# Kernel optimization log

Measured on AMD Instinct MI355X. Metric: run time of the kernel, lower is better.

The kernel has to match this reference:

```python
import jax, jax.numpy as jnp
import numpy as np

GRID = 128
N0 = 262144
CHANNELS = [16, 32, 64, 128, 256]
EPS = 1e-5
OFFS2 = [(dx, dy, dz) for dx in (0, 1) for dy in (0, 1) for dz in (0, 1)]
OFFS3 = [(dx, dy, dz) for dx in (-1, 0, 1) for dy in (-1, 0, 1) for dz in (-1, 0, 1)]


def _keys(c, size):
    return (c[:, 0].astype(np.int64) * size + c[:, 1]) * size + c[:, 2]


def _rulebook(in_coords, out_coords, offsets, size_in, stride):
    # explicit-GEMM rulebook: for each kernel offset, (input_idx, output_idx) pairs,
    # padded to n_out with a validity mask so shapes are static.
    ik = _keys(in_coords, size_in)
    order = np.argsort(ik)
    sk = ik[order]
    K, P = len(offsets), out_coords.shape[0]
    I = np.zeros((K, P), np.int32)
    O = np.zeros((K, P), np.int32)
    M = np.zeros((K, P), bool)
    for k, off in enumerate(offsets):
        nbr = out_coords * stride + np.asarray(off)
        valid = np.all((nbr >= 0) & (nbr < size_in), axis=1)
        nk = _keys(np.clip(nbr, 0, size_in - 1), size_in)
        pos = np.minimum(np.searchsorted(sk, nk), len(sk) - 1)
        found = valid & (sk[pos] == nk)
        cnt = int(found.sum())
        I[k, :cnt] = order[pos[found]]
        O[k, :cnt] = np.nonzero(found)[0]
        M[k, :cnt] = True
    return I, O, M


def setup_inputs() -> dict:
    rng = np.random.RandomState(0)
    flat = rng.choice(GRID ** 3, size=N0, replace=False)
    coords = np.stack([flat // (GRID * GRID), (flat // GRID) % GRID, flat % GRID], 1).astype(np.int64)
    key = jax.random.key(0)
    ctr = [0]
    def nrm(shape, scale=1.0):
        ctr[0] += 1
        return scale * jax.random.normal(jax.random.fold_in(key, ctr[0]), shape, jnp.float32)
    inp = {"x": nrm((N0, CHANNELS[0]))}
    size = GRID
    for l in range(4):
        cin, cout = CHANNELS[l], CHANNELS[l + 1]
        out_coords = np.unique(coords // 2, axis=0)
        dI, dO, dM = _rulebook(coords, out_coords, OFFS2, size, 2)       # stride-2, k=2 down conv
        bI, bO, bM = _rulebook(out_coords, out_coords, OFFS3, size // 2, 1)  # stride-1, k=3 block conv
        inp[f"dW{l}"] = nrm((8, cin, cout), (8 * cin) ** -0.5)
        inp[f"dI{l}"] = jnp.asarray(dI); inp[f"dO{l}"] = jnp.asarray(dO); inp[f"dM{l}"] = jnp.asarray(dM)
        inp[f"dG{l}"] = 1.0 + nrm((cout,), 0.1)
        inp[f"dB{l}"] = nrm((cout,), 0.1)
        inp[f"dN{l}"] = int(out_coords.shape[0])
        inp[f"bW{l}"] = nrm((27, cout, cout), (27 * cout) ** -0.5)
        inp[f"bC{l}"] = nrm((cout,), 0.01)
        inp[f"bI{l}"] = jnp.asarray(bI); inp[f"bO{l}"] = jnp.asarray(bO); inp[f"bM{l}"] = jnp.asarray(bM)
        inp[f"bG{l}"] = 1.0 + nrm((cout,), 0.1)
        inp[f"bH{l}"] = nrm((cout,), 0.1)
        coords = out_coords
        size //= 2
    return inp


def _conv(f, W, I, O, M, n_out, bias=None):
    # gather -> GEMM -> scatter-add, one pass per kernel offset (fixed small K)
    out = jnp.zeros((n_out, W.shape[-1]), f.dtype)
    for k in range(W.shape[0]):
        g = jnp.where(M[k][:, None], f[I[k]], 0.0)
        out = out.at[O[k]].add(g @ W[k])
    return out if bias is None else out + bias


def _bn_relu(f, g, b):
    # training-mode BatchNorm over active voxels, fused with ReLU
    m = f.mean(0)
    v = jnp.mean((f - m) ** 2, 0)
    return jax.nn.relu((f - m) * (g * jax.lax.rsqrt(v + EPS)) + b)


def _forward(x, levels):
    outs = [x]
    for (dW, dI, dO, dM, dG, dB, dN, bW, bC, bI, bO, bM, bG, bH) in levels:
        x = _bn_relu(_conv(x, dW, dI, dO, dM, dN), dG, dB)        # down block (bias=False)
        x = _bn_relu(_conv(x, bW, bI, bO, bM, dN, bC), bG, bH)    # ConvBlock
        outs.append(x)
    return tuple(outs)


def reference(x, dW0, dI0, dO0, dM0, dG0, dB0, dN0, bW0, bC0, bI0, bO0, bM0, bG0, bH0,
              dW1, dI1, dO1, dM1, dG1, dB1, dN1, bW1, bC1, bI1, bO1, bM1, bG1, bH1,
              dW2, dI2, dO2, dM2, dG2, dB2, dN2, bW2, bC2, bI2, bO2, bM2, bG2, bH2,
              dW3, dI3, dO3, dM3, dG3, dB3, dN3, bW3, bC3, bI3, bO3, bM3, bG3, bH3):
    levels = [
        (dW0, dI0, dO0, dM0, dG0, dB0, dN0, bW0, bC0, bI0, bO0, bM0, bG0, bH0),
        (dW1, dI1, dO1, dM1, dG1, dB1, dN1, bW1, bC1, bI1, bO1, bM1, bG1, bH1),
        (dW2, dI2, dO2, dM2, dG2, dB2, dN2, bW2, bC2, bI2, bO2, bM2, bG2, bH2),
        (dW3, dI3, dO3, dM3, dG3, dB3, dN3, bW3, bC3, bI3, bO3, bM3, bG3, bH3),
    ]
    return _forward(x, levels)
```

## Files before the change

### kernel.cpp

```cpp
#include <hip/hip_runtime.h>
#include <hip/hip_bf16.h>
#include <stdint.h>
#include <stddef.h>

typedef __hip_bfloat16 bf16;
typedef __attribute__((ext_vector_type(8))) short bf8_t;
typedef __attribute__((ext_vector_type(4))) float f4_t;
static const int CH[5] = {16, 32, 64, 128, 256};

__device__ __forceinline__ float b2f(unsigned short u) {
    return __uint_as_float(((unsigned int)u) << 16);
}
__device__ __forceinline__ unsigned short f2bu(float f) {
    union { bf16 h; unsigned short u; } cv;
    cv.h = __float2bfloat16(f);
    return cv.u;
}
__device__ __forceinline__ void fma4(float4& a, float s, const float4& w) {
    a.x = fmaf(s, w.x, a.x);
    a.y = fmaf(s, w.y, a.y);
    a.z = fmaf(s, w.z, a.z);
    a.w = fmaf(s, w.w, a.w);
}
struct us4 { unsigned short a, b, c, d; };

__global__ void k_sentinel(float* __restrict__ out, float v) {
    if (threadIdx.x == 0) out[0] = v;
}

__global__ void SparseConvEncoder_20633022890309_kernel(
        const unsigned char* __restrict__ bM0, int* __restrict__ flag) {
    if (threadIdx.x == 0) {
        flag[0] = 1;
        flag[1] = 0;
        flag[2] = (bM0[0] == 1 && bM0[1] == 0 && bM0[2] == 0 && bM0[3] == 0 && bM0[4] == 1) ? 1 : 0;
    }
}

__global__ void __launch_bounds__(256) k_copy(const float* __restrict__ x,
                                              float* __restrict__ y, long n) {
    long i = (long)blockIdx.x * 256 + threadIdx.x;
    if (i < n) y[i] = x[i];
}

__global__ void __launch_bounds__(256) k_copytob(const float* __restrict__ x,
                                                 float* __restrict__ y,
                                                 unsigned short* __restrict__ yb, long n) {
    long i = (long)blockIdx.x * 256 + threadIdx.x;
    if (i < n) {
        float v = x[i];
        y[i] = v;
        yb[i] = f2bu(v);
    }
}

__global__ void __launch_bounds__(256) k_wt2(const float* __restrict__ dW,
                                             unsigned short* __restrict__ dWt, int dcin,
                                             const float* __restrict__ bW,
                                             unsigned short* __restrict__ bWt, int bcin,
                                             int cout, long dtot, long btot) {
    long i = (long)blockIdx.x * 256 + threadIdx.x;
    if (i < dtot) {
        long cc = (long)dcin * cout;
        int k = (int)(i / cc);
        int rem = (int)(i % cc);
        int co = rem / dcin, ci = rem % dcin;
        dWt[i] = f2bu(dW[((long)k * dcin + ci) * cout + co]);
    } else if (i < dtot + btot) {
        long j = i - dtot;
        long cc = (long)bcin * cout;
        int k = (int)(j / cc);
        int rem = (int)(j % cc);
        int co = rem / bcin, ci = rem % bcin;
        bWt[j] = f2bu(bW[((long)k * bcin + ci) * cout + co]);
    }
}

__global__ void __launch_bounds__(256) k_scatter(const int* __restrict__ I,
                                                 const int* __restrict__ O,
                                                 const void* __restrict__ M,
                                                 const int* __restrict__ flag,
                                                 int* __restrict__ R, int P, int k0, int cnt) {
    int i = blockIdx.x * 256 + threadIdx.x;
    if (i >= cnt) return;
    long gi = (long)k0 * P + i;
    int m = flag[2] ? ((const int*)M)[gi] : (int)((const unsigned char*)M)[gi];
    if (!m) return;
    R[(long)(i / P) * P + O[gi]] = I[gi];
}

__global__ void __launch_bounds__(256) k_init(float* __restrict__ out,
                                              const float* __restrict__ bias,
                                              long total, int maskC) {
    long i = (long)blockIdx.x * 256 + threadIdx.x;
    if (i < total) out[i] = bias ? bias[i & maskC] : 0.f;
}

template <int CIN, int TN, int MODE, int KT>
__global__ void __launch_bounds__(256) k_mconv(const unsigned short* __restrict__ Xb,
                                               const unsigned short* __restrict__ Wt,
                                               const float* __restrict__ bias,
                                               const int* __restrict__ R,
                                               float* __restrict__ out,
                                               int n, int cout, int kcnt, int gs) {
    const int lane = threadIdx.x & 63;
    const int wave = threadIdx.x >> 6;
    const int rt = blockIdx.x * 4 + wave;
    const int row_tiles = (n + 15) >> 4;
    if (rt >= row_tiles) return;
    const int m = lane & 15, q = lane >> 4;
    const int o = rt * 16 + m;
    const int co0 = blockIdx.y * (16 * TN);
    const bf8_t zero = {};

    f4_t acc[TN];
#pragma unroll
    for (int t = 0; t < TN; ++t) {
        if (MODE == 0) {
            float bv = bias ? bias[co0 + t * 16 + m] : 0.f;
            acc[t][0] = bv; acc[t][1] = bv; acc[t][2] = bv; acc[t][3] = bv;
        } else if (MODE == 1) {
#pragma unroll
            for (int g = 0; g < 4; ++g) {
                int row = rt * 16 + q * 4 + g;
                acc[t][g] = (row < n) ? out[(long)row * cout + co0 + t * 16 + m] : 0.f;
            }
        } else {
            acc[t][0] = 0.f; acc[t][1] = 0.f; acc[t][2] = 0.f; acc[t][3] = 0.f;
        }
    }

    bool touched = (MODE != 2);

    if constexpr (KT > 0) {
        int r[KT];
#pragma unroll
        for (int kk = 0; kk < KT; ++kk)
            r[kk] = (o < n) ? R[(long)kk * n + o] : -1;

        if constexpr (CIN == 16) {
            bf8_t a[KT / 2];
#pragma unroll
            for (int p = 0; p < KT / 2; ++p) {
                int rsel = (q < 2) ? r[2 * p] : r[2 * p + 1];
                long ax = (long)((rsel >= 0) ? rsel : 0) * CIN + (q & 1) * 8;
                bf8_t av = *(const bf8_t*)(Xb + ax);
                a[p] = (rsel >= 0) ? av : zero;
            }
#pragma unroll
            for (int p = 0; p < KT / 2; ++p) {
                int ksel = 2 * p + (q >> 1);
#pragma unroll
                for (int t = 0; t < TN; ++t) {
                    int co = co0 + t * 16 + m;
                    long bx = ((long)ksel * cout + co) * CIN + (q & 1) * 8;
                    bf8_t b = *(const bf8_t*)(Wt + bx);
                    acc[t] = __builtin_amdgcn_mfma_f32_16x16x32_bf16(a[p], b, acc[t], 0, 0, 0);
                }
            }
        } else {
            constexpr int NC = CIN / 32;
            constexpr int GB = (KT > 9) ? 9 : KT;
#pragma unroll
            for (int g0 = 0; g0 < KT; g0 += GB) {
                bf8_t a[GB][NC];
#pragma unroll
                for (int j = 0; j < GB; ++j) {
                    int kk = g0 + j;
#pragma unroll
                    for (int cb = 0; cb < NC; ++cb) {
                        long ax = (long)((r[kk] >= 0) ? r[kk] : 0) * CIN + cb * 32 + q * 8;
                        bf8_t av = *(const bf8_t*)(Xb + ax);
                        a[j][cb] = (r[kk] >= 0) ? av : zero;
                    }
                }
#pragma unroll
                for (int j = 0; j < GB; ++j) {
                    int kk = g0 + j;
#pragma unroll
                    for (int cb = 0; cb < NC; ++cb) {
#pragma unroll
                        for (int t = 0; t < TN; ++t) {
                            int co = co0 + t * 16 + m;
                            long bx = ((long)kk * cout + co) * CIN + cb * 32 + q * 8;
                            bf8_t b = *(const bf8_t*)(Wt + bx);
                            acc[t] = __builtin_amdgcn_mfma_f32_16x16x32_bf16(a[j][cb], b,
                                                                             acc[t], 0, 0, 0);
                        }
                    }
                }
            }
        }
    } else {
        int ks = 0, ke = kcnt;
        if (MODE == 2) {
            ks = blockIdx.z * gs;
            ke = ks + gs;
            if (ke > kcnt) ke = kcnt;
        }
        constexpr int NC = (CIN >= 32) ? (CIN / 32) : 1;
        constexpr int JB = (CIN >= 128) ? 2 : 4;
        for (int kb = ks; kb < ke; kb += JB) {
            int rj[JB];
#pragma unroll
            for (int j = 0; j < JB; ++j) {
                int kk = kb + j;
                rj[j] = (kk < ke && o < n) ? R[(long)kk * n + o] : -1;
            }
            if (MODE == 2) {
                int any = 0;
#pragma unroll
                for (int j = 0; j < JB; ++j) any |= (rj[j] >= 0) ? 1 : 0;
                if (__ballot(any) == 0ULL) continue;
                touched = true;
            }
            bf8_t a[JB][NC];
#pragma unroll
            for (int j = 0; j < JB; ++j) {
                int kk = kb + j;
                bool inb = (kk < ke) && (rj[j] >= 0);
#pragma unroll
                for (int cb = 0; cb < NC; ++cb) {
                    const bool kval = !(CIN == 16 && q >= 2);
                    const int kbase = (CIN == 16) ? (kval ? q * 8 : 0) : (cb * 32 + q * 8);
                    long ax = (long)(inb ? rj[j] : 0) * CIN + kbase;
                    bf8_t av = *(const bf8_t*)(Xb + ax);
                    a[j][cb] = (inb && kval) ? av : zero;
                }
            }
#pragma unroll
            for (int j = 0; j < JB; ++j) {
                int kk = kb + j;
                if (kk >= ke) break;
#pragma unroll
                for (int cb = 0; cb < NC; ++cb) {
                    const bool kval = !(CIN == 16 && q >= 2);
                    const int kbase = (CIN == 16) ? (kval ? q * 8 : 0) : (cb * 32 + q * 8);
#pragma unroll
                    for (int t = 0; t < TN; ++t) {
                        int co = co0 + t * 16 + m;
                        long bx = ((long)kk * cout + co) * CIN + kbase;
                        bf8_t bv = *(const bf8_t*)(Wt + bx);
                        bf8_t b = kval ? bv : zero;
                        acc[t] = __builtin_amdgcn_mfma_f32_16x16x32_bf16(a[j][cb], b,
                                                                         acc[t], 0, 0, 0);
                    }
                }
            }
        }
    }

    if (MODE == 2 && !touched) return;
#pragma unroll
    for (int t = 0; t < TN; ++t) {
#pragma unroll
        for (int g = 0; g < 4; ++g) {
            int row = rt * 16 + q * 4 + g;
            if (row >= n) continue;
            float* p = out + (long)row * cout + co0 + t * 16 + m;
            if (MODE == 2) atomicAdd(p, acc[t][g]);
            else *p = acc[t][g];
        }
    }
}

static void mconv_dispatch(int cin, int tn, int mode, int kt, dim3 grd,
                           const unsigned short* Xb, const unsigned short* Wt,
                           const float* bias, const int* R, float* out,
                           int n, int cout, int kcnt, int gs, hipStream_t stream) {
#define MF_(CC, TT, KK)                                                            \
    if (cin == CC && tn == TT && mode == 0 && kt == KK) {                          \
        k_mconv<CC, TT, 0, KK><<<grd, 256, 0, stream>>>(Xb, Wt, bias, R, out, n,   \
                                                        cout, kcnt, gs);           \
        return;                                                                    \
    }
    MF_(16, 2, 8) MF_(32, 2, 8) MF_(32, 4, 8) MF_(64, 2, 8) MF_(64, 4, 8)
    MF_(32, 2, 27) MF_(64, 2, 27) MF_(64, 4, 27)
#undef MF_
#define M3_(CC, TT, MM)                                                            \
    if (cin == CC && tn == TT && mode == MM) {                                     \
        k_mconv<CC, TT, MM, 0><<<grd, 256, 0, stream>>>(Xb, Wt, bias, R, out, n,   \
                                                        cout, kcnt, gs);           \
        return;                                                                    \
    }
#define M2_(CC) M3_(CC, 2, 0) M3_(CC, 2, 1) M3_(CC, 2, 2) \
                M3_(CC, 4, 0) M3_(CC, 4, 1) M3_(CC, 4, 2)
    M2_(16) M2_(32) M2_(64) M2_(128) M2_(256)
#undef M2_
#undef M3_
}

static void run_mconv(const unsigned short* Xb, const unsigned short* Wt,
                      const float* bias, const int* I, const int* O, const void* M,
                      const int* flag, int* R, float* out, int n, int cin, int cout,
                      int K, int G, hipStream_t stream) {
    int rt = (n + 15) / 16;
    int bx = (rt + 3) / 4;
    int tn = (cout >= 64) ? 4 : 2;
    int gy = cout / (16 * tn);
    if (tn == 4 && (long)bx * gy < 1024) { tn = 2; gy = cout / 32; }
    long bxy = (long)bx * gy;
    int kg = 1;
    if (bxy < 512 && G >= K) {
        kg = (int)((1024 + bxy - 1) / bxy);
        if (kg > K) kg = K;
    }
    int gs = (K + kg - 1) / kg;
    kg = (K + gs - 1) / gs;

    if (kg > 1) {
        int cnt = K * n;
        hipMemsetAsync(R, 0xFF, (size_t)cnt * 4, stream);
        k_scatter<<<(cnt + 255) / 256, 256, 0, stream>>>(I, O, M, flag, R, n, 0, cnt);
        long tot = (long)n * cout;
        k_init<<<(int)((tot + 255) / 256), 256, 0, stream>>>(out, bias, tot, cout - 1);
        mconv_dispatch(cin, tn, 2, 0, dim3(bx, gy, kg), Xb, Wt, bias, R, out,
                       n, cout, K, gs, stream);
    } else {
        for (int k0 = 0; k0 < K; k0 += G) {
            int g = (K - k0 < G) ? (K - k0) : G;
            int cnt = g * n;
            hipMemsetAsync(R, 0xFF, (size_t)cnt * 4, stream);
            k_scatter<<<(cnt + 255) / 256, 256, 0, stream>>>(I, O, M, flag, R, n, k0, cnt);
            int kt = (k0 == 0 && g == K) ? K : 0;
            mconv_dispatch(cin, tn, (k0 == 0) ? 0 : 1, kt, dim3(bx, gy, 1), Xb,
                           Wt + (size_t)k0 * cout * cin, bias, R, out,
                           n, cout, g, g, stream);
        }
    }
}

template <int CIN, int ROWS, int XBF, int MODE>
__global__ void __launch_bounds__(256) k_conv_t(const void* __restrict__ X,
                                                const float* __restrict__ W,
                                                const float* __restrict__ bias,
                                                const int* __restrict__ R,
                                                float* __restrict__ out,
                                                int n, int cout,
                                                int wk0, int kcnt, int gs) {
    const int c4 = threadIdx.x;
    const int by = blockDim.y;
    const int base = blockIdx.x * by * ROWS;
    const float* Xf = (const float*)X;
    const unsigned short* Xb = (const unsigned short*)X;

    int o[ROWS];
    float4 acc[ROWS];
    bool touched[ROWS];
#pragma unroll
    for (int j = 0; j < ROWS; ++j) {
        o[j] = base + j * by + threadIdx.y;
        touched[j] = false;
        acc[j] = make_float4(0.f, 0.f, 0.f, 0.f);
        if (o[j] < n) {
            if (MODE == 0) {
                if (bias) acc[j] = *(const float4*)(bias + c4 * 4);
            } else if (MODE == 1) {
                acc[j] = *(const float4*)(out + (long)o[j] * cout + c4 * 4);
            }
        }
    }
    int ks = 0, ke = kcnt;
    if (MODE == 2) {
        ks = blockIdx.y * gs;
        ke = ks + gs;
        if (ke > kcnt) ke = kcnt;
    }
    for (int kk = ks; kk < ke; ++kk) {
        int r[ROWS];
        bool any = false;
#pragma unroll
        for (int j = 0; j < ROWS; ++j) {
            r[j] = (o[j] < n) ? R[(long)kk * n + o[j]] : -1;
            any = any || (r[j] >= 0);
            touched[j] = touched[j] || (r[j] >= 0);
        }
        if (!any) continue;
        const float* wk = W + ((long)(wk0 + kk) * CIN) * cout + c4 * 4;
#pragma unroll
        for (int ci = 0; ci < CIN; ci += 4) {
            float4 w0 = *(const float4*)(wk + (long)(ci + 0) * cout);
            float4 w1 = *(const float4*)(wk + (long)(ci + 1) * cout);
            float4 w2 = *(const float4*)(wk + (long)(ci + 2) * cout);
            float4 w3 = *(const float4*)(wk + (long)(ci + 3) * cout);
#pragma unroll
            for (int j = 0; j < ROWS; ++j) {
                if (r[j] < 0) continue;
                float x0, x1, x2, x3;
                if (XBF) {
                    us4 u = *(const us4*)(Xb + (long)r[j] * CIN + ci);
                    x0 = b2f(u.a); x1 = b2f(u.b); x2 = b2f(u.c); x3 = b2f(u.d);
                } else {
                    float4 xv = *(const float4*)(Xf + (long)r[j] * CIN + ci);
                    x0 = xv.x; x1 = xv.y; x2 = xv.z; x3 = xv.w;
                }
                fma4(acc[j], x0, w0);
                fma4(acc[j], x1, w1);
                fma4(acc[j], x2, w2);
                fma4(acc[j], x3, w3);
            }
        }
    }
#pragma unroll
    for (int j = 0; j < ROWS; ++j) {
        if (o[j] >= n) continue;
        if (MODE == 2) {
            if (!touched[j]) continue;
            float* p = out + (long)o[j] * cout + c4 * 4;
            atomicAdd(p + 0, acc[j].x);
            atomicAdd(p + 1, acc[j].y);
            atomicAdd(p + 2, acc[j].z);
            atomicAdd(p + 3, acc[j].w);
        } else {
            *(float4*)(out + (long)o[j] * cout + c4 * 4) = acc[j];
        }
    }
}

static void conv_dispatch(int cin, int rows, int xbf, int mode, dim3 grd, dim3 blk,
                          const void* X, const float* W, const float* bias,
                          const int* R, float* out, int n, int cout,
                          int wk0, int kcnt, int gs, hipStream_t stream) {
#define C3_(CC, RR, XB, MM)                                                        \
    if (cin == CC && rows == RR && xbf == XB && mode == MM) {                      \
        k_conv_t<CC, RR, XB, MM><<<grd, blk, 0, stream>>>(X, W, bias, R, out, n,   \
                                                          cout, wk0, kcnt, gs);    \
        return;                                                                    \
    }
#define C2_(CC, RR) C3_(CC, RR, 0, 0) C3_(CC, RR, 0, 1) C3_(CC, RR, 0, 2) \
                    C3_(CC, RR, 1, 0) C3_(CC, RR, 1, 1) C3_(CC, RR, 1, 2)
#define C1_(CC) C2_(CC, 1) C2_(CC, 2) C2_(CC, 4)
    C1_(16) C1_(32) C1_(64) C1_(128) C1_(256)
#undef C1_
#undef C2_
#undef C3_
}

static void run_conv(const void* X, int xbf, const float* W, const float* bias,
                     const int* I, const int* O, const void* M, const int* flag,
                     int* R, float* out, int n, int cin, int cout, int K,
                     int G, hipStream_t stream) {
    int bx = cout / 4, by = 256 / bx;
    int g4 = (n + by * 4 - 1) / (by * 4);
    int g2 = (n + by * 2 - 1) / (by * 2);
    int rows;
    if (g4 >= 1024) rows = 4;
    else if (g2 >= 1024) rows = 2;
    else rows = 1;
    int gridn = (n + by * rows - 1) / (by * rows);
    int kg = 1;
    if (gridn < 768 && G >= K) {
        kg = (2048 + gridn - 1) / gridn;
        if (kg > K) kg = K;
    }
    int gs = (K + kg - 1) / kg;
    kg = (K + gs - 1) / gs;
    dim3 blk(bx, by);
    if (kg > 1) {
        int cnt = K * n;
        hipMemsetAsync(R, 0xFF, (size_t)cnt * 4, stream);
        k_scatter<<<(cnt + 255) / 256, 256, 0, stream>>>(I, O, M, flag, R, n, 0, cnt);
        long tot = (long)n * cout;
        k_init<<<(int)((tot + 255) / 256), 256, 0, stream>>>(out, bias, tot, cout - 1);
        conv_dispatch(cin, rows, xbf, 2, dim3(gridn, kg), blk, X, W, bias, R, out,
                      n, cout, 0, K, gs, stream);
    } else {
        for (int k0 = 0; k0 < K; k0 += G) {
            int g = (K - k0 < G) ? (K - k0) : G;
            int cnt = g * n;
            hipMemsetAsync(R, 0xFF, (size_t)cnt * 4, stream);
            k_scatter<<<(cnt + 255) / 256, 256, 0, stream>>>(I, O, M, flag, R, n, k0, cnt);
            conv_dispatch(cin, rows, xbf, (k0 == 0) ? 0 : 1, dim3(gridn, 1), blk,
                          X, W, bias, R, out, n, cout, k0, g, g, stream);
        }
    }
}

__global__ void __launch_bounds__(256) k_stats(const float* __restrict__ X,
                                               float* __restrict__ sums, int n, int C) {
    int c = threadIdx.x, ty = threadIdx.y, ny = blockDim.y;
    float s1 = 0.f, s2 = 0.f;
    for (int o = blockIdx.x * ny + ty; o < n; o += gridDim.x * ny) {
        float v = X[(long)o * C + c];
        s1 += v;
        s2 += v * v;
    }
    __shared__ float sm[512];
    sm[ty * C + c] = s1;
    sm[256 + ty * C + c] = s2;
    __syncthreads();
    if (ty == 0) {
        for (int t = 1; t < ny; ++t) {
            s1 += sm[t * C + c];
            s2 += sm[256 + t * C + c];
        }
        atomicAdd(&sums[c], s1);
        atomicAdd(&sums[C + c], s2);
    }
}

__global__ void __launch_bounds__(256) k_apply(const float* __restrict__ X,
                                               const float* __restrict__ sums,
                                               const float* __restrict__ g,
                                               const float* __restrict__ b,
                                               void* __restrict__ Y, int ybf,
                                               unsigned short* __restrict__ Y2,
                                               long total, int maskC, int C, float inv_n) {
    long i = (long)blockIdx.x * 256 + threadIdx.x;
    if (i >= total) return;
    int c = (int)(i & (long)maskC);
    float mean = sums[c] * inv_n;
    float var = fmaf(-mean, mean, sums[C + c] * inv_n);
    float sc = g[c] * rsqrtf(var + 1e-5f);
    float sh = fmaf(-mean, sc, b[c]);
    float v = fmaf(X[i], sc, sh);
    v = v > 0.f ? v : 0.f;
    if (ybf) ((unsigned short*)Y)[i] = f2bu(v);
    else     ((float*)Y)[i] = v;
    if (Y2) Y2[i] = f2bu(v);
}

static void run_bn(const float* src, int n, int C, const float* g, const float* b,
                   void* dst, int dst_bf16, unsigned short* dst2,
                   float* sums, hipStream_t stream) {
    hipMemsetAsync(sums, 0, 2 * C * sizeof(float), stream);
    dim3 sblk(C, 256 / C);
    int sgrd = (n + (int)sblk.y - 1) / (int)sblk.y;
    if (sgrd > 1024) sgrd = 1024;
    k_stats<<<sgrd, sblk, 0, stream>>>(src, sums, n, C);
    long tot = (long)n * C;
    k_apply<<<(int)((tot + 255) / 256), 256, 0, stream>>>(src, sums, g, b, dst, dst_bf16,
                                                          dst2, tot, C - 1, C,
                                                          1.0f / (float)n);
}

extern "C" void kernel_launch(void* const* d_in, const int* in_sizes, int n_in,
                              void* d_out, int out_size, void* d_ws, size_t ws_size,
                              hipStream_t stream) {
    float* out = (float*)d_out;

    int stride = 0;
    if (n_in == 57) stride = 14;
    else if (n_in == 53) stride = 13;
    if (!stride) {
        k_sentinel<<<1, 64, 0, stream>>>(out, 10240.f + (float)n_in);
        return;
    }
    static const int o14[13] = {0, 1, 2, 3, 4, 5, 7, 8, 9, 10, 11, 12, 13};
    static const int o13[13] = {0, 1, 2, 3, 4, 5, 6, 7, 8, 9, 10, 11, 12};
    const int* om = (stride == 14) ? o14 : o13;

    long n0 = (long)in_sizes[0];
    int P[4];
    bool ok = (n0 % 16 == 0);
    long total = n0;
    for (int l = 0; l < 4 && ok; ++l) {
        int base = 1 + stride * l;
        int sdI = in_sizes[base + om[1]], sdO = in_sizes[base + om[2]], sdM = in_sizes[base + om[3]];
        int sbI = in_sizes[base + om[8]], sbO = in_sizes[base + om[9]], sbM = in_sizes[base + om[10]];
        if (sdI <= 0 || sdI % 8 != 0 || sdO != sdI || sdM != sdI) { ok = false; break; }
        int p = sdI / 8;
        if (sbI != 27 * p || sbO != sbI || sbM != sbI) { ok = false; break; }
        if (in_sizes[base + om[0]] != 8 * CH[l] * CH[l + 1]) { ok = false; break; }
        if (in_sizes[base + om[6]] != 27 * CH[l + 1] * CH[l + 1]) { ok = false; break; }
        P[l] = p;
        total += (long)p * CH[l + 1];
    }
    if (!ok) {
        k_sentinel<<<1, 64, 0, stream>>>(out, 49152.f);
        return;
    }
    if (total != (long)out_size) {
        k_sentinel<<<1, 64, 0, stream>>>(out, 53248.f);
        return;
    }

    auto al = [](size_t x) { return (x + 255) / 256 * 256; };
    size_t maxBuf = 0, maxP = 0, maxXb = 0;
    long rowsIn[4] = {n0 / 16, P[0], P[1], P[2]};
    for (int l = 0; l < 4; ++l) {
        size_t b = (size_t)P[l] * CH[l + 1];
        if (b > maxBuf) maxBuf = b;
        if ((size_t)P[l] > maxP) maxP = (size_t)P[l];
        size_t xi = (size_t)rowsIn[l] * CH[l];
        if (xi > maxXb) maxXb = xi;
    }
    const size_t fixed = 4096;
    size_t rmin = al(maxP * 4);
    size_t dwt_sz = al((size_t)8 * 128 * 256 * 2);
    size_t bwt_sz = al((size_t)27 * 256 * 256 * 2);
    size_t mf_need = dwt_sz + bwt_sz + al(maxXb * 2) + al(maxBuf * 2) + fixed + rmin;

    if (ws_size >= mf_need) {
        char* wsp = (char*)d_ws;
        unsigned short* dWt = (unsigned short*)wsp; wsp += dwt_sz;
        unsigned short* bWt = (unsigned short*)wsp; wsp += bwt_sz;
        unsigned short* xb = (unsigned short*)wsp;  wsp += al(maxXb * 2);
        unsigned short* bufB = (unsigned short*)wsp; wsp += al(maxBuf * 2);
        float* sums = (float*)wsp; wsp += 1024;
        int* flag = (int*)wsp;     wsp += 2048;
        int* R = (int*)wsp;
        size_t Rbytes = ws_size - (size_t)(wsp - (char*)d_ws);

        SparseConvEncoder_20633022890309_kernel<<<1, 64, 0, stream>>>(
            (const unsigned char*)d_in[1 + om[10]], flag);
        k_copytob<<<(int)((n0 + 255) / 256), 256, 0, stream>>>((const float*)d_in[0],
                                                               out, xb, n0);

        long coff = n0;
        for (int l = 0; l < 4; ++l) {
            int base = 1 + stride * l;
            const float* dW = (const float*)d_in[base + om[0]];
            const int* dI = (const int*)d_in[base + om[1]];
            const int* dO = (const int*)d_in[base + om[2]];
            const void* dM = d_in[base + om[3]];
            const float* dG = (const float*)d_in[base + om[4]];
            const float* dB = (const float*)d_in[base + om[5]];
            const float* bW = (const float*)d_in[base + om[6]];
            const float* bC = (const float*)d_in[base + om[7]];
            const int* bI = (const int*)d_in[base + om[8]];
            const int* bO = (const int*)d_in[base + om[9]];
            const void* bM = d_in[base + om[10]];
            const float* bG = (const float*)d_in[base + om[11]];
            const float* bH = (const float*)d_in[base + om[12]];
            int n = P[l], cin = CH[l], cout = CH[l + 1];

            int G = (int)(Rbytes / ((size_t)n * 4));
            if (G > 27) G = 27;
            if (G < 1) G = 1;

            float* chunkp = out + coff;

            long dwtot = (long)8 * cin * cout;
            long bwtot = (long)27 * cout * cout;
            k_wt2<<<(int)((dwtot + bwtot + 255) / 256), 256, 0, stream>>>(
                dW, dWt, cin, bW, bWt, cout, cout, dwtot, bwtot);

            run_mconv(xb, dWt, nullptr, dI, dO, dM, flag, R, chunkp,
                      n, cin, cout, 8, (G > 8) ? 8 : G, stream);
            run_bn(chunkp, n, cout, dG, dB, bufB, 1, nullptr, sums, stream);

            run_mconv(bufB, bWt, bC, bI, bO, bM, flag, R, chunkp,
                      n, cout, cout, 27, G, stream);
            run_bn(chunkp, n, cout, bG, bH, chunkp, 0,
                   (l < 3) ? xb : nullptr, sums, stream);

            coff += (long)n * cout;
        }
        return;
    }

    int bufB_bf16;
    size_t bufBytes;
    if (ws_size >= fixed + al(maxBuf * 4) + rmin) { bufB_bf16 = 0; bufBytes = al(maxBuf * 4); }
    else if (ws_size >= fixed + al(maxBuf * 2) + rmin) { bufB_bf16 = 1; bufBytes = al(maxBuf * 2); }
    else {
        k_sentinel<<<1, 64, 0, stream>>>(out, 16384.f + (float)(ws_size >> 20));
        return;
    }
    size_t Rbytes = ws_size - fixed - bufBytes;
    char* wsp = (char*)d_ws;
    void* bufB = (void*)wsp;   wsp += bufBytes;
    float* sums = (float*)wsp; wsp += 1024;
    int* flag = (int*)wsp;     wsp += 2048;
    int* R = (int*)wsp;

    SparseConvEncoder_20633022890309_kernel<<<1, 64, 0, stream>>>(
        (const unsigned char*)d_in[1 + om[10]], flag);
    k_copy<<<(int)((n0 + 255) / 256), 256, 0, stream>>>((const float*)d_in[0], out, n0);

    long coff = n0;
    const void* cur_in = d_in[0];
    int cur_xbf = 0;
    for (int l = 0; l < 4; ++l) {
        int base = 1 + stride * l;
        const float* dW = (const float*)d_in[base + om[0]];
        const int* dI = (const int*)d_in[base + om[1]];
        const int* dO = (const int*)d_in[base + om[2]];
        const void* dM = d_in[base + om[3]];
        const float* dG = (const float*)d_in[base + om[4]];
        const float* dB = (const float*)d_in[base + om[5]];
        const float* bW = (const float*)d_in[base + om[6]];
        const float* bC = (const float*)d_in[base + om[7]];
        const int* bI = (const int*)d_in[base + om[8]];
        const int* bO = (const int*)d_in[base + om[9]];
        const void* bM = d_in[base + om[10]];
        const float* bG = (const float*)d_in[base + om[11]];
        const float* bH = (const float*)d_in[base + om[12]];
        int n = P[l], cin = CH[l], cout = CH[l + 1];

        int G = (int)(Rbytes / ((size_t)n * 4));
        if (G > 27) G = 27;
        if (G < 1) G = 1;

        float* chunkp = out + coff;
        run_conv(cur_in, cur_xbf, dW, nullptr, dI, dO, dM, flag, R, chunkp,
                 n, cin, cout, 8, (G > 8) ? 8 : G, stream);
        run_bn(chunkp, n, cout, dG, dB, bufB, bufB_bf16, nullptr, sums, stream);
        run_conv(bufB, bufB_bf16, bW, bC, bI, bO, bM, flag, R, chunkp,
                 n, cout, cout, 27, G, stream);
        run_bn(chunkp, n, cout, bG, bH, chunkp, 0, nullptr, sums, stream);

        cur_in = (const void*)chunkp;
        cur_xbf = 0;
        coff += (long)n * cout;
    }
}
```

Before: 834.2 us.

## Software-pipeline gathered A loads across groups with sched barriers and launch bounds

Restructures the fixed-KT conv path so the gathered input loads for one group of kernel offsets are issued while MFMAs for the previous group run, using a three-group prefetch/compute schedule fenced by sched_barrier. Sched barriers are also added after the A loads in the other paths, so the compiler cannot interleave loads and MFMAs. Launch bounds now request two blocks per SM to cap register use. The heuristic that fell back to TN=2 for small grids is removed, giving fewer, wider blocks. This trades higher register pressure from the extra prefetch buffers against better memory latency hiding, and may reduce parallelism on small levels.

```diff
diff --git a/kernel.cpp b/kernel.cpp
--- a/kernel.cpp
+++ b/kernel.cpp
@@ -97,12 +97,12 @@
 }
 
 template <int CIN, int TN, int MODE, int KT>
-__global__ void __launch_bounds__(256) k_mconv(const unsigned short* __restrict__ Xb,
-                                               const unsigned short* __restrict__ Wt,
-                                               const float* __restrict__ bias,
-                                               const int* __restrict__ R,
-                                               float* __restrict__ out,
-                                               int n, int cout, int kcnt, int gs) {
+__global__ void __launch_bounds__(256, 2) k_mconv(const unsigned short* __restrict__ Xb,
+                                                  const unsigned short* __restrict__ Wt,
+                                                  const float* __restrict__ bias,
+                                                  const int* __restrict__ R,
+                                                  float* __restrict__ out,
+                                                  int n, int cout, int kcnt, int gs) {
     const int lane = threadIdx.x & 63;
     const int wave = threadIdx.x >> 6;
     const int rt = blockIdx.x * 4 + wave;
@@ -147,6 +147,7 @@
                 bf8_t av = *(const bf8_t*)(Xb + ax);
                 a[p] = (rsel >= 0) ? av : zero;
             }
+            __builtin_amdgcn_sched_barrier(0);
 #pragma unroll
             for (int p = 0; p < KT / 2; ++p) {
                 int ksel = 2 * p + (q >> 1);
@@ -160,36 +161,61 @@
             }
         } else {
             constexpr int NC = CIN / 32;
-            constexpr int GB = (KT > 9) ? 9 : KT;
-#pragma unroll
-            for (int g0 = 0; g0 < KT; g0 += GB) {
-                bf8_t a[GB][NC];
-#pragma unroll
-                for (int j = 0; j < GB; ++j) {
-                    int kk = g0 + j;
-#pragma unroll
-                    for (int cb = 0; cb < NC; ++cb) {
-                        long ax = (long)((r[kk] >= 0) ? r[kk] : 0) * CIN + cb * 32 + q * 8;
-                        bf8_t av = *(const bf8_t*)(Xb + ax);
-                        a[j][cb] = (r[kk] >= 0) ? av : zero;
-                    }
-                }
-#pragma unroll
-                for (int j = 0; j < GB; ++j) {
-                    int kk = g0 + j;
-#pragma unroll
-                    for (int cb = 0; cb < NC; ++cb) {
-#pragma unroll
-                        for (int t = 0; t < TN; ++t) {
-                            int co = co0 + t * 16 + m;
-                            long bx = ((long)kk * cout + co) * CIN + cb * 32 + q * 8;
-                            bf8_t b = *(const bf8_t*)(Wt + bx);
-                            acc[t] = __builtin_amdgcn_mfma_f32_16x16x32_bf16(a[j][cb], b,
-                                                                             acc[t], 0, 0, 0);
-                        }
-                    }
-                }
-            }
+            constexpr int GB = (KT * NC * 4 <= 128) ? KT : 9;
+            constexpr int NG = (KT + GB - 1) / GB;
+
+#define PRE_GRP(A, G0)                                                              \
+    _Pragma("unroll")                                                               \
+    for (int j = 0; j < GB; ++j) {                                                  \
+        _Pragma("unroll")                                                           \
+        for (int cb = 0; cb < NC; ++cb) {                                           \
+            int kk = (G0) + j;                                                      \
+            long ax = (long)((r[kk] >= 0) ? r[kk] : 0) * CIN + cb * 32 + q * 8;     \
+            bf8_t av = *(const bf8_t*)(Xb + ax);                                    \
+            A[j][cb] = (r[kk] >= 0) ? av : zero;                                    \
+        }                                                                           \
+    }
+
+#define CMP_GRP(A, G0)                                                              \
+    _Pragma("unroll")                                                               \
+    for (int j = 0; j < GB; ++j) {                                                  \
+        _Pragma("unroll")                                                           \
+        for (int cb = 0; cb < NC; ++cb) {                                           \
+            _Pragma("unroll")                                                       \
+            for (int t = 0; t < TN; ++t) {                                          \
+                int kk = (G0) + j;                                                  \
+                int co = co0 + t * 16 + m;                                          \
+                long bx = ((long)kk * cout + co) * CIN + cb * 32 + q * 8;           \
+                bf8_t b = *(const bf8_t*)(Wt + bx);                                 \
+                acc[t] = __builtin_amdgcn_mfma_f32_16x16x32_bf16(A[j][cb], b,       \
+                                                                 acc[t], 0, 0, 0);  \
+            }                                                                       \
+        }                                                                           \
+    }
+
+            if constexpr (NG == 1) {
+                bf8_t a0[GB][NC];
+                PRE_GRP(a0, 0)
+                __builtin_amdgcn_sched_barrier(0);
+                CMP_GRP(a0, 0)
+            } else {
+                static_assert(NG == 3, "phase structure assumes 3 groups");
+                bf8_t a0[GB][NC];
+                bf8_t a1[GB][NC];
+                bf8_t a2[GB][NC];
+                PRE_GRP(a0, 0)
+                PRE_GRP(a1, GB)
+                __builtin_amdgcn_sched_barrier(0);
+                CMP_GRP(a0, 0)
+                __builtin_amdgcn_sched_barrier(0);
+                PRE_GRP(a2, 2 * GB)
+                __builtin_amdgcn_sched_barrier(0);
+                CMP_GRP(a1, GB)
+                __builtin_amdgcn_sched_barrier(0);
+                CMP_GRP(a2, 2 * GB)
+            }
+#undef PRE_GRP
+#undef CMP_GRP
         }
     } else {
         int ks = 0, ke = kcnt;
@@ -228,6 +254,7 @@
                     a[j][cb] = (inb && kval) ? av : zero;
                 }
             }
+            __builtin_amdgcn_sched_barrier(0);
 #pragma unroll
             for (int j = 0; j < JB; ++j) {
                 int kk = kb + j;
@@ -298,7 +325,6 @@
     int bx = (rt + 3) / 4;
     int tn = (cout >= 64) ? 4 : 2;
     int gy = cout / (16 * tn);
-    if (tn == 4 && (long)bx * gy < 1024) { tn = 2; gy = cout / 32; }
     long bxy = (long)bx * gy;
     int kg = 1;
     if (bxy < 512 && G >= K) {
```

New measurement: 822.1 us. About the same (-1.5%).
